# Optimization experiments

Measured on AMD Instinct MI355X. Metric: run time of the kernel, lower is better.

Reference implementation:

```python
import jax, jax.numpy as jnp
import numpy as np

B, N, DIM, HEADS = 4, 1024, 1024, 16
DH = DIM // HEADS
SCALE = 1.0 / np.sqrt(DH)
EPS = 1e-6


def clinear(x, Wr, Wi, br, bi):
    # (a+bi)(Wr+Wi i): real = a Wr^T - b Wi^T, imag = a Wi^T + b Wr^T
    xr, xi = x.real, x.imag
    real = xr @ Wr.T - xi @ Wi.T + br
    imag = xr @ Wi.T + xi @ Wr.T + bi
    return jax.lax.complex(real, imag)


def cln(x, gamma, beta):
    # normalize magnitude over last dim, keep phase
    mag = jnp.abs(x)
    phase = jnp.angle(x)
    mean = jnp.mean(mag, axis=-1, keepdims=True)
    var = jnp.var(mag, axis=-1, keepdims=True)
    nm = (mag - mean) / jnp.sqrt(var + EPS)
    nm = nm * gamma + beta
    return jax.lax.complex(nm * jnp.cos(phase), nm * jnp.sin(phase))


def forward(xr, xi, Wq_r, Wq_i, bq_r, bq_i, Wk_r, Wk_i, bk_r, bk_i,
            Wv_r, Wv_i, bv_r, bv_i, Wo_r, Wo_i, bo_r, bo_i,
            gq, beq, gk, bek, gv, bev):
    x = jax.lax.complex(xr, xi)  # [B,N,D] complex64

    def heads(t):
        return t.reshape(B, N, HEADS, DH).transpose(0, 2, 1, 3)  # [B,H,N,dh]

    Q = heads(cln(clinear(x, Wq_r, Wq_i, bq_r, bq_i), gq, beq))
    K = heads(cln(clinear(x, Wk_r, Wk_i, bk_r, bk_i), gk, bek))
    V = heads(cln(clinear(x, Wv_r, Wv_i, bv_r, bv_i), gv, bev))

    Qf = jnp.fft.fft(Q, axis=2, norm='ortho')
    Kf = jnp.fft.fft(K, axis=2, norm='ortho')
    Vf = jnp.fft.fft(V, axis=2, norm='ortho')

    scores = jnp.einsum('bhnd,bhmd->bhnm', Qf, jnp.conj(Kf)) * SCALE
    attn = jax.nn.softmax(scores.real, axis=-1)  # real-valued softmax
    # attn is real; multiply into complex Vf componentwise
    out_f = jax.lax.complex(jnp.einsum('bhnm,bhmd->bhnd', attn, Vf.real),
                            jnp.einsum('bhnm,bhmd->bhnd', attn, Vf.imag))
    out = jnp.fft.ifft(out_f, axis=2, norm='ortho')
    out = out.transpose(0, 2, 1, 3).reshape(B, N, DIM)
    y = clinear(out, Wo_r, Wo_i, bo_r, bo_i)
    # return real||imag concatenated on last axis (float32 view of complex output)
    return jnp.concatenate([y.real, y.imag], axis=-1)


def setup_inputs() -> dict:
    key = jax.random.key(0)
    ks = jax.random.split(key, 16)
    wscale = np.sqrt(2.0 / (DIM + DIM)).astype(np.float32)
    d = {}
    d['xr'] = jax.random.normal(ks[0], (B, N, DIM), jnp.float32)
    d['xi'] = jax.random.normal(ks[1], (B, N, DIM), jnp.float32)
    i = 2
    for name in ('q', 'k', 'v', 'o'):
        d[f'W{name}_r'] = jax.random.normal(ks[i], (DIM, DIM), jnp.float32) * wscale; i += 1
        d[f'W{name}_i'] = jax.random.normal(ks[i], (DIM, DIM), jnp.float32) * wscale; i += 1
        d[f'b{name}_r'] = jnp.zeros((DIM,), jnp.float32)
        d[f'b{name}_i'] = jnp.zeros((DIM,), jnp.float32)
    for name in ('q', 'k', 'v'):
        d[f'g{name}'] = jnp.ones((DIM,), jnp.float32)
        d[f'be{name}'] = jnp.zeros((DIM,), jnp.float32)
    return d


def reference(xr, xi, Wq_r, Wq_i, bq_r, bq_i, Wk_r, Wk_i, bk_r, bk_i,
              Wv_r, Wv_i, bv_r, bv_i, Wo_r, Wo_i, bo_r, bo_i,
              gq, beq, gk, bek, gv, bev):
    return forward(xr, xi, Wq_r, Wq_i, bq_r, bq_i, Wk_r, Wk_i, bk_r, bk_i,
                   Wv_r, Wv_i, bv_r, bv_i, Wo_r, Wo_i, bo_r, bo_i,
                   gq, beq, gk, bek, gv, bev)
```

## Files before the change

kernel.cpp:

```cpp
#include <hip/hip_runtime.h>
#include <math.h>

#define BB 4
#define NN 1024
#define DIMM 1024
#define HHH 16
#define DHH 64
#define BN 4096
#define EPS_LN 1e-6f

typedef __bf16 bf16_t;
typedef __bf16 bf16x8 __attribute__((ext_vector_type(8)));
typedef float f32x4 __attribute__((ext_vector_type(4)));
typedef float f32x16 __attribute__((ext_vector_type(16)));
#define MFMA16(a, b, c) __builtin_amdgcn_mfma_f32_16x16x32_bf16(a, b, c, 0, 0, 0)
#define MFMA32(a, b, c) __builtin_amdgcn_mfma_f32_32x32x16_bf16(a, b, c, 0, 0, 0)
#define AS1 __attribute__((address_space(1)))
#define AS3 __attribute__((address_space(3)))

__device__ inline unsigned pk2(float a, float b) {
  union { bf16_t h[2]; unsigned u; } c;
  c.h[0] = (bf16_t)a; c.h[1] = (bf16_t)b;
  return c.u;
}
union U16 { uint4 u; bf16x8 v; };

__global__ __launch_bounds__(256) void pack_x(
    const float* __restrict__ xr, const float* __restrict__ xi,
    bf16_t* __restrict__ out)
{
  int t = blockIdx.x * 256 + threadIdx.x;
  size_t e = (size_t)t * 8;
  int row = (int)(e >> 11), col = (int)(e & 2047);
  const float* src = (col < 1024) ? (xr + (size_t)row * 1024 + col)
                                  : (xi + (size_t)row * 1024 + col - 1024);
  float4 a = *(const float4*)src;
  float4 b = *(const float4*)(src + 4);
  bf16x8 o;
  o[0] = (bf16_t)a.x; o[1] = (bf16_t)a.y; o[2] = (bf16_t)a.z; o[3] = (bf16_t)a.w;
  o[4] = (bf16_t)b.x; o[5] = (bf16_t)b.y; o[6] = (bf16_t)b.z; o[7] = (bf16_t)b.w;
  *(bf16x8*)(out + e) = o;
}

__global__ __launch_bounds__(256) void pack_w(
    const float* __restrict__ Wr, const float* __restrict__ Wi,
    const float* __restrict__ br, const float* __restrict__ bi,
    bf16_t* __restrict__ Wcat, float* __restrict__ bcat)
{
  int t = blockIdx.x * 256 + threadIdx.x;
  size_t e = (size_t)t * 8;
  int row = (int)(e >> 11), col = (int)(e & 2047);
  const float* src;
  float sgn = 1.f;
  if (row < 1024) {
    if (col < 1024) src = Wr + (size_t)row * 1024 + col;
    else          { src = Wi + (size_t)row * 1024 + col - 1024; sgn = -1.f; }
  } else {
    int r2 = row - 1024;
    if (col < 1024) src = Wi + (size_t)r2 * 1024 + col;
    else            src = Wr + (size_t)r2 * 1024 + col - 1024;
  }
  float4 a = *(const float4*)src;
  float4 b = *(const float4*)(src + 4);
  bf16x8 o;
  o[0] = (bf16_t)(sgn * a.x); o[1] = (bf16_t)(sgn * a.y);
  o[2] = (bf16_t)(sgn * a.z); o[3] = (bf16_t)(sgn * a.w);
  o[4] = (bf16_t)(sgn * b.x); o[5] = (bf16_t)(sgn * b.y);
  o[6] = (bf16_t)(sgn * b.z); o[7] = (bf16_t)(sgn * b.w);
  *(bf16x8*)(Wcat + e) = o;
  if (e < 2048) {
#pragma unroll
    for (int j = 0; j < 8; ++j) {
      int n = (int)e + j;
      bcat[n] = (n < 1024) ? br[n] : bi[n - 1024];
    }
  }
}

__global__ __launch_bounds__(256) void gemm_bf16(
    const bf16_t* __restrict__ A, const bf16_t* __restrict__ Bt,
    const float* __restrict__ bias,
    float* __restrict__ Cr, float* __restrict__ Ci, int ldc)
{
  __shared__ bf16_t sA[128 * 64];
  __shared__ bf16_t sB[128 * 64];
  const int tid = threadIdx.x;
  const int w = tid >> 6, l = tid & 63;
  const int lo4 = l & 15, hi = l >> 4;
  const int wr = w >> 1, wc = w & 1;
  const int row0 = blockIdx.y * 128, col0 = blockIdx.x * 128;

  const int srow = (l >> 3);
  const int scol = (l & 7) * 8;
  const bf16_t* gA[4];
  const bf16_t* gB[4];
#pragma unroll
  for (int i = 0; i < 4; ++i) {
    int r = (w * 4 + i) * 8 + srow;
    gA[i] = A  + (size_t)(row0 + r) * 2048 + scol;
    gB[i] = Bt + (size_t)(col0 + r) * 2048 + scol;
  }

  f32x4 acc[4][4] = {};
  for (int k0 = 0; k0 < 2048; k0 += 64) {
    __syncthreads();
#pragma unroll
    for (int i = 0; i < 4; ++i) {
      __builtin_amdgcn_global_load_lds((const AS1 void*)(gA[i] + k0),
                                       (AS3 void*)&sA[(w * 4 + i) * 512], 16, 0, 0);
      __builtin_amdgcn_global_load_lds((const AS1 void*)(gB[i] + k0),
                                       (AS3 void*)&sB[(w * 4 + i) * 512], 16, 0, 0);
    }
    __syncthreads();
#pragma unroll
    for (int kk = 0; kk < 2; ++kk) {
      bf16x8 am[4], bn[4];
#pragma unroll
      for (int i = 0; i < 4; ++i)
        am[i] = *(const bf16x8*)&sA[(wr * 64 + i * 16 + lo4) * 64 + kk * 32 + hi * 8];
#pragma unroll
      for (int j = 0; j < 4; ++j)
        bn[j] = *(const bf16x8*)&sB[(wc * 64 + j * 16 + lo4) * 64 + kk * 32 + hi * 8];
#pragma unroll
      for (int i = 0; i < 4; ++i)
#pragma unroll
        for (int j = 0; j < 4; ++j)
          acc[i][j] = MFMA16(am[i], bn[j], acc[i][j]);
    }
  }
  const int colg0 = col0 + wc * 64;
  float* Cp = (colg0 < 1024) ? Cr : Ci;
  const int cb = colg0 & 1023;
#pragma unroll
  for (int i = 0; i < 4; ++i) {
#pragma unroll
    for (int j = 0; j < 4; ++j) {
      float bv = bias[colg0 + j * 16 + lo4];
#pragma unroll
      for (int r = 0; r < 4; ++r) {
        int rowg = row0 + wr * 64 + i * 16 + hi * 4 + r;
        Cp[(size_t)rowg * ldc + cb + j * 16 + lo4] = acc[i][j][r] + bv;
      }
    }
  }
}

__global__ __launch_bounds__(256) void ln_stats(
    const float* __restrict__ re, const float* __restrict__ im,
    float2* __restrict__ st)
{
  __shared__ float red[8];
  const int row = blockIdx.x;
  const int tid = threadIdx.x;
  const float* pr = re + (size_t)row * DIMM;
  const float* pi = im + (size_t)row * DIMM;
  float s = 0.f, s2 = 0.f;
#pragma unroll
  for (int t = 0; t < 4; ++t) {
    int c = tid + t * 256;
    float vr = pr[c], vi = pi[c];
    float mg = sqrtf(vr * vr + vi * vi);
    s += mg; s2 += mg * mg;
  }
#pragma unroll
  for (int o = 32; o; o >>= 1) { s += __shfl_down(s, o); s2 += __shfl_down(s2, o); }
  if ((tid & 63) == 0) { red[tid >> 6] = s; red[4 + (tid >> 6)] = s2; }
  __syncthreads();
  if (tid == 0) {
    float S = red[0] + red[1] + red[2] + red[3];
    float S2 = red[4] + red[5] + red[6] + red[7];
    float mean = S * (1.f / DIMM);
    float var = S2 * (1.f / DIMM) - mean * mean;
    st[row] = make_float2(mean, rsqrtf(var + EPS_LN));
  }
}

#define LIDX(d_, c_) (((d_) << 10) + ((c_) ^ (((c_) >> 5) & 31) ^ (((d_) & 7) << 2)))

__global__ __launch_bounds__(512) void fft_kernel(
    const float* __restrict__ inR, const float* __restrict__ inI,
    bf16_t* __restrict__ outR, bf16_t* __restrict__ outI,
    int in_sb, int in_sh, int in_sn, int in_sd,
    int out_sb, int out_sh, int out_sn,
    float sign, float oscale, int imode, int omode,
    const float2* __restrict__ stats,
    const float* __restrict__ gamma, const float* __restrict__ beta)
{
  __shared__ float lr[8 * 1024], li[8 * 1024];
  __shared__ float2 tw[1024];
  const int tid = threadIdx.x;
  const int dc = blockIdx.x & 7;
  const int bh = blockIdx.x >> 3;
  const int b = bh >> 4, h = bh & 15;
  const float* bR = inR + (size_t)b * in_sb + (size_t)h * in_sh;
  const float* bI = inI + (size_t)b * in_sb + (size_t)h * in_sh;
#pragma unroll
  for (int t = tid; t < 1024; t += 512) {
    float ang = sign * 3.14159265358979323846f * (float)t * (1.f / 512.f);
    float sn, cs;
    __sincosf(ang, &sn, &cs);
    tw[t] = make_float2(cs, sn);
  }
  if (imode == 0) {
    float gg[8], bb[8];
    if (stats) {
#pragma unroll
      for (int ds = 0; ds < 8; ++ds) {
        gg[ds] = gamma[h * DHH + dc * 8 + ds];
        bb[ds] = beta[h * DHH + dc * 8 + ds];
      }
    }
#pragma unroll
    for (int rep = 0; rep < 2; ++rep) {
      int n = tid + rep * 512;
      const float* pR = bR + (size_t)n * in_sn + dc * 8;
      const float* pI = bI + (size_t)n * in_sn + dc * 8;
      union { float4 q[2]; float f[8]; } ur, ui;
      ur.q[0] = *(const float4*)pR;      ur.q[1] = *(const float4*)(pR + 4);
      ui.q[0] = *(const float4*)pI;      ui.q[1] = *(const float4*)(pI + 4);
      if (stats) {
        float2 stv = stats[b * NN + n];
#pragma unroll
        for (int ds = 0; ds < 8; ++ds) {
          float a = ur.f[ds], c2 = ui.f[ds];
          float mag = sqrtf(a * a + c2 * c2);
          float nm = (mag - stv.x) * stv.y * gg[ds] + bb[ds];
          if (mag > 0.f) { float sc = nm / mag; ur.f[ds] = a * sc; ui.f[ds] = c2 * sc; }
          else           { ur.f[ds] = nm; ui.f[ds] = 0.f; }
        }
      }
#pragma unroll
      for (int ds = 0; ds < 8; ++ds) {
        int ax = LIDX(ds, n);
        lr[ax] = ur.f[ds];
        li[ax] = ui.f[ds];
      }
    }
  } else {
    const int ds = tid & 7, nb = tid >> 3;
    const float* pR = bR + (size_t)(dc * 8 + ds) * in_sd + nb * 16;
    const float* pI = bI + (size_t)(dc * 8 + ds) * in_sd + nb * 16;
#pragma unroll
    for (int k = 0; k < 16; k += 4) {
      float4 v = *(const float4*)(pR + k);
      float4 w = *(const float4*)(pI + k);
      int c = nb * 16 + k;
      lr[LIDX(ds, c + 0)] = v.x;  li[LIDX(ds, c + 0)] = w.x;
      lr[LIDX(ds, c + 1)] = v.y;  li[LIDX(ds, c + 1)] = w.y;
      lr[LIDX(ds, c + 2)] = v.z;  li[LIDX(ds, c + 2)] = w.z;
      lr[LIDX(ds, c + 3)] = v.w;  li[LIDX(ds, c + 3)] = w.w;
    }
  }
  __syncthreads();
  const int dsub = tid & 7;
  const int jb = tid >> 3;
  int lq2 = 8;
  for (int st = 0; st < 5; ++st) {
    const int qtr = 1 << lq2;
    const int tmul = 1 << (2 * st);
    for (int jt = 0; jt < 4; ++jt) {
      int j = jb + jt * 64;
      int o = j & (qtr - 1);
      int i0 = ((j >> lq2) << (lq2 + 2)) + o;
      int a0 = LIDX(dsub, i0);
      int a1 = LIDX(dsub, i0 + qtr);
      int a2 = LIDX(dsub, i0 + 2 * qtr);
      int a3 = LIDX(dsub, i0 + 3 * qtr);
      float x0r = lr[a0], x0i = li[a0];
      float x1r = lr[a1], x1i = li[a1];
      float x2r = lr[a2], x2i = li[a2];
      float x3r = lr[a3], x3i = li[a3];
      float ar = x0r + x2r, ai2 = x0i + x2i;
      float br = x0r - x2r, bi  = x0i - x2i;
      float cr = x1r + x3r, ci  = x1i + x3i;
      float dr = x1r - x3r, di  = x1i - x3i;
      float2 t1 = tw[o * tmul];
      float2 t2 = tw[2 * o * tmul];
      float2 t3 = tw[3 * o * tmul];
      lr[a0] = ar + cr;  li[a0] = ai2 + ci;
      float u1r = br - sign * di, u1i = bi + sign * dr;
      lr[a1] = u1r * t1.x - u1i * t1.y;  li[a1] = u1r * t1.y + u1i * t1.x;
      float u2r = ar - cr, u2i = ai2 - ci;
      lr[a2] = u2r * t2.x - u2i * t2.y;  li[a2] = u2r * t2.y + u2i * t2.x;
      float u3r = br + sign * di, u3i = bi - sign * dr;
      lr[a3] = u3r * t3.x - u3i * t3.y;  li[a3] = u3r * t3.y + u3i * t3.x;
    }
    __syncthreads();
    lq2 -= 2;
  }
  bf16_t* oRb = outR + (size_t)b * out_sb + (size_t)h * out_sh;
  bf16_t* oIb = outI + (size_t)b * out_sb + (size_t)h * out_sh;
#pragma unroll
  for (int rep = 0; rep < 2; ++rep) {
    int n = tid + rep * 512;
    int rv2 = __brev((unsigned)n) >> 22;
    int p = ((rv2 & 0x155) << 1) | ((rv2 >> 1) & 0x155);
    float fr[8], fi[8];
#pragma unroll
    for (int ds = 0; ds < 8; ++ds) {
      fr[ds] = lr[LIDX(ds, p)] * oscale;
      fi[ds] = li[LIDX(ds, p)] * oscale;
    }
    if (omode == 1) {
      size_t tb = (size_t)(n >> 5) * 4096;
#pragma unroll
      for (int ds = 0; ds < 8; ++ds) {
        int dch = dc * 8 + ds;
        size_t ga = tb + (size_t)dch * 32 + ((n & 31) ^ (((dch >> 1) & 3) << 3));
        oRb[ga] = (bf16_t)fr[ds];
        oIb[ga] = (bf16_t)fi[ds];
      }
    } else {
      int cb = dc * 8;
      if (omode == 2) cb = (dc ^ (n & 7)) * 8;
      bf16x8 v0, w0;
#pragma unroll
      for (int k = 0; k < 8; ++k) {
        v0[k] = (bf16_t)fr[k];
        w0[k] = (bf16_t)fi[k];
      }
      size_t gb = (size_t)n * out_sn + cb;
      *(bf16x8*)(oRb + gb) = v0;
      *(bf16x8*)(oIb + gb) = w0;
    }
  }
}

__global__ __launch_bounds__(256, 2) void fattn(
    const bf16_t* __restrict__ Qf, const bf16_t* __restrict__ Kfs,
    const bf16_t* __restrict__ Vfs, float* __restrict__ OT)
{
  __shared__ bf16_t K3[3][4096];
  __shared__ bf16_t V3[3][4096];
  const int tid = threadIdx.x;
  const int w = tid >> 6, l = tid & 63;
  const int lq = l & 31;
  const int h = l >> 5;
  const int i = blockIdx.x;
  const int j = i >> 3;
  const int bh = (i & 7) * 8 + (j >> 3);
  const int q0 = (j & 7) * 128 + w * 32;

  bf16x8 bq[8];
  const bf16_t* qp = Qf + ((size_t)bh * NN + q0 + lq) * 128 + h * 8;
#pragma unroll
  for (int kk = 0; kk < 8; ++kk) bq[kk] = *(const bf16x8*)(qp + kk * 16);

  f32x16 o[4] = {};
  float m = -3e38f, ln = 0.f;

  const bf16_t* kg = Kfs + (size_t)bh * 131072 + w * 1024 + l * 8;
  const bf16_t* vg = Vfs + (size_t)bh * 131072 + w * 1024 + l * 8;
  const int kswz = (lq & 7) << 3;
  const int vswz = ((lq >> 1) & 3) << 3;

#pragma unroll
  for (int tt = 0; tt < 2; ++tt) {
    const bf16_t* kt = kg + (size_t)tt * 4096;
    const bf16_t* vt = vg + (size_t)tt * 4096;
#pragma unroll
    for (int ii = 0; ii < 2; ++ii) {
      __builtin_amdgcn_global_load_lds((const AS1 void*)(kt + ii * 512),
                                       (AS3 void*)&K3[tt][w * 1024 + ii * 512], 16, 0, 0);
      __builtin_amdgcn_global_load_lds((const AS1 void*)(vt + ii * 512),
                                       (AS3 void*)&V3[tt][w * 1024 + ii * 512], 16, 0, 0);
    }
  }
  asm volatile("s_waitcnt vmcnt(4)" ::: "memory");
  __builtin_amdgcn_s_barrier();
  __builtin_amdgcn_sched_barrier(0);

  int cur = 0;
  for (int t = 0; t < 32; ++t) {
    if (t < 30) {
      int nb = cur + 2; if (nb >= 3) nb -= 3;
      const bf16_t* kt = kg + (size_t)(t + 2) * 4096;
      const bf16_t* vt = vg + (size_t)(t + 2) * 4096;
#pragma unroll
      for (int ii = 0; ii < 2; ++ii) {
        __builtin_amdgcn_global_load_lds((const AS1 void*)(kt + ii * 512),
                                         (AS3 void*)&K3[nb][w * 1024 + ii * 512], 16, 0, 0);
        __builtin_amdgcn_global_load_lds((const AS1 void*)(vt + ii * 512),
                                         (AS3 void*)&V3[nb][w * 1024 + ii * 512], 16, 0, 0);
      }
    }

    f32x16 s = {};
#pragma unroll
    for (int kk = 0; kk < 8; ++kk) {
      bf16x8 ak = *(const bf16x8*)&K3[cur][lq * 128 + ((kk * 16 + h * 8) ^ kswz)];
      s = MFMA32(ak, bq[kk], s);
    }

    float pmax = s[0];
#pragma unroll
    for (int r = 1; r < 16; ++r) pmax = fmaxf(pmax, s[r]);
    pmax = fmaxf(pmax, __shfl_xor(pmax, 32));
    if (!__all(pmax - m <= 8.f)) {
      float mnew = fmaxf(m, pmax);
      float alpha = __expf(m - mnew);
      m = mnew;
      ln *= alpha;
#pragma unroll
      for (int db = 0; db < 4; ++db)
#pragma unroll
        for (int r = 0; r < 16; ++r) o[db][r] *= alpha;
    }
    float pf[16];
    float rs = 0.f;
#pragma unroll
    for (int r = 0; r < 16; ++r) { pf[r] = __expf(s[r] - m); rs += pf[r]; }
    rs += __shfl_xor(rs, 32);
    ln += rs;

    unsigned pw[8];
#pragma unroll
    for (int ii = 0; ii < 8; ++ii) pw[ii] = pk2(pf[2 * ii], pf[2 * ii + 1]);
    unsigned r0 = (unsigned)__shfl_xor((int)(h ? pw[0] : pw[2]), 32);
    unsigned r1 = (unsigned)__shfl_xor((int)(h ? pw[1] : pw[3]), 32);
    unsigned r2 = (unsigned)__shfl_xor((int)(h ? pw[4] : pw[6]), 32);
    unsigned r3 = (unsigned)__shfl_xor((int)(h ? pw[5] : pw[7]), 32);
    U16 bp0, bp1;
    bp0.u.x = h ? r0 : pw[0];  bp0.u.y = h ? r1 : pw[1];
    bp0.u.z = h ? pw[2] : r0;  bp0.u.w = h ? pw[3] : r1;
    bp1.u.x = h ? r2 : pw[4];  bp1.u.y = h ? r3 : pw[5];
    bp1.u.z = h ? pw[6] : r2;  bp1.u.w = h ? pw[7] : r3;

#pragma unroll
    for (int db = 0; db < 4; ++db) {
      int r = db * 32 + lq;
      bf16x8 av0 = *(const bf16x8*)&V3[cur][r * 32 + ((h * 8) ^ vswz)];
      bf16x8 av1 = *(const bf16x8*)&V3[cur][r * 32 + ((16 + h * 8) ^ vswz)];
      o[db] = MFMA32(av0, bp0.v, o[db]);
      o[db] = MFMA32(av1, bp1.v, o[db]);
    }

    if (t < 31) {
      if (t < 30) asm volatile("s_waitcnt vmcnt(4)" ::: "memory");
      else        asm volatile("s_waitcnt vmcnt(0)" ::: "memory");
      __builtin_amdgcn_s_barrier();
      __builtin_amdgcn_sched_barrier(0);
    }
    cur = (cur == 2) ? 0 : cur + 1;
  }

  float inv = 1.f / ln;
  const size_t otb = (size_t)bh * 128 * NN + q0 + lq;
#pragma unroll
  for (int db = 0; db < 4; ++db)
#pragma unroll
    for (int r = 0; r < 16; ++r) {
      int dl = (r & 3) + 8 * (r >> 2) + 4 * h;
      OT[otb + (size_t)(db * 32 + dl) * NN] = o[db][r] * inv;
    }
}

extern "C" void kernel_launch(void* const* d_in, const int* in_sizes, int n_in,
                              void* d_out, int out_size, void* d_ws, size_t ws_size,
                              hipStream_t stream) {
  const float* xr   = (const float*)d_in[0];
  const float* xi   = (const float*)d_in[1];
  const float* Wqr  = (const float*)d_in[2];
  const float* Wqi  = (const float*)d_in[3];
  const float* bqr  = (const float*)d_in[4];
  const float* bqi  = (const float*)d_in[5];
  const float* Wkr  = (const float*)d_in[6];
  const float* Wki  = (const float*)d_in[7];
  const float* bkr  = (const float*)d_in[8];
  const float* bki  = (const float*)d_in[9];
  const float* Wvr  = (const float*)d_in[10];
  const float* Wvi  = (const float*)d_in[11];
  const float* bvr  = (const float*)d_in[12];
  const float* bvi  = (const float*)d_in[13];
  const float* Wor  = (const float*)d_in[14];
  const float* Woi  = (const float*)d_in[15];
  const float* bor  = (const float*)d_in[16];
  const float* boi  = (const float*)d_in[17];
  const float* gq   = (const float*)d_in[18];
  const float* beq  = (const float*)d_in[19];
  const float* gk   = (const float*)d_in[20];
  const float* bek  = (const float*)d_in[21];
  const float* gv   = (const float*)d_in[22];
  const float* bev  = (const float*)d_in[23];

  char* wp = (char*)d_ws;
  bf16_t* Axaug = (bf16_t*)wp;  wp += (size_t)4096 * 2048 * 2;
  bf16_t* Wcat  = (bf16_t*)wp;  wp += (size_t)2048 * 2048 * 2;
  float*  bcat  = (float*)wp;   wp += (size_t)2048 * 4;
  float2* lnst  = (float2*)wp;  wp += (size_t)4096 * 8;
  float*  Ar    = (float*)wp;   wp += (size_t)4096 * 1024 * 4;
  float*  Ai    = (float*)wp;   wp += (size_t)4096 * 1024 * 4;
  bf16_t* Qf    = (bf16_t*)wp;  wp += (size_t)64 * 1024 * 128 * 2;
  bf16_t* Kf    = (bf16_t*)wp;  wp += (size_t)64 * 1024 * 128 * 2;
  bf16_t* VfT   = (bf16_t*)wp;  wp += (size_t)64 * 1024 * 128 * 2;
  bf16_t* Yaug  = Qf;
  float*  OT    = Ar;

  const dim3 gGemm(16, 32);
  const int gPackX = (4096 * 2048 / 8) / 256;
  const int gPackW = (2048 * 2048 / 8) / 256;
  const int gFft = 64 * 8;
  const int gAtt = 64 * 8;

  pack_x<<<gPackX, 256, 0, stream>>>(xr, xi, Axaug);

  pack_w<<<gPackW, 256, 0, stream>>>(Wqr, Wqi, bqr, bqi, Wcat, bcat);
  gemm_bf16<<<gGemm, 256, 0, stream>>>(Axaug, Wcat, bcat, Ar, Ai, 1024);
  ln_stats<<<BN, 256, 0, stream>>>(Ar, Ai, lnst);
  fft_kernel<<<gFft, 512, 0, stream>>>(Ar, Ai, Qf, Qf + 64,
      NN * DIMM, DHH, DIMM, 1,
      16 * NN * 128, NN * 128, 128,
      -1.0f, 0.03125f * 0.125f, 0, 0, lnst, gq, beq);
  pack_w<<<gPackW, 256, 0, stream>>>(Wkr, Wki, bkr, bki, Wcat, bcat);
  gemm_bf16<<<gGemm, 256, 0, stream>>>(Axaug, Wcat, bcat, Ar, Ai, 1024);
  ln_stats<<<BN, 256, 0, stream>>>(Ar, Ai, lnst);
  fft_kernel<<<gFft, 512, 0, stream>>>(Ar, Ai, Kf, Kf + 64,
      NN * DIMM, DHH, DIMM, 1,
      16 * NN * 128, NN * 128, 128,
      -1.0f, 0.03125f, 0, 2, lnst, gk, bek);
  pack_w<<<gPackW, 256, 0, stream>>>(Wvr, Wvi, bvr, bvi, Wcat, bcat);
  gemm_bf16<<<gGemm, 256, 0, stream>>>(Axaug, Wcat, bcat, Ar, Ai, 1024);
  ln_stats<<<BN, 256, 0, stream>>>(Ar, Ai, lnst);
  fft_kernel<<<gFft, 512, 0, stream>>>(Ar, Ai, VfT, VfT + 2048,
      NN * DIMM, DHH, DIMM, 1,
      16 * 131072, 131072, 0,
      -1.0f, 0.03125f, 0, 1, lnst, gv, bev);
  fattn<<<gAtt, 256, 0, stream>>>(Qf, Kf, VfT, OT);
  fft_kernel<<<gFft, 512, 0, stream>>>(OT, OT + (size_t)64 * NN, Yaug, Yaug + 1024,
      16 * 128 * NN, 128 * NN, 1, NN,
      NN * 2048, 64, 2048,
      +1.0f, 0.03125f, 1, 0, nullptr, nullptr, nullptr);
  float* yout = (float*)d_out;
  pack_w<<<gPackW, 256, 0, stream>>>(Wor, Woi, bor, boi, Wcat, bcat);
  gemm_bf16<<<gGemm, 256, 0, stream>>>(Yaug, Wcat, bcat, yout, yout + 1024, 2048);
}
```

Before: 431.4 us.

## Fuse Q/K/V projections into one GEMM and store intermediates in bf16

Replaces three separate projection GEMMs and three LN-stat passes with a single 6144-wide QKV GEMM and one batched stats kernel. The projection output and the attention output OT are now stored as bf16 instead of fp32, roughly halving intermediate memory traffic for the FFT and stats kernels. This cuts launch count and gives the GEMM a larger grid, which should fill the device better. The cost is extra rounding of pre-layernorm activations and attention outputs to bf16, plus a larger workspace.

```diff
diff --git a/kernel.cpp b/kernel.cpp
--- a/kernel.cpp
+++ b/kernel.cpp
@@ -11,6 +11,7 @@
 
 typedef __bf16 bf16_t;
 typedef __bf16 bf16x8 __attribute__((ext_vector_type(8)));
+typedef __bf16 bf16x4 __attribute__((ext_vector_type(4)));
 typedef float f32x4 __attribute__((ext_vector_type(4)));
 typedef float f32x16 __attribute__((ext_vector_type(16)));
 #define MFMA16(a, b, c) __builtin_amdgcn_mfma_f32_16x16x32_bf16(a, b, c, 0, 0, 0)
@@ -77,6 +78,71 @@
   }
 }
 
+__global__ __launch_bounds__(256) void gemm_qkv(
+    const bf16_t* __restrict__ A, const bf16_t* __restrict__ Bt,
+    const float* __restrict__ bias, bf16_t* __restrict__ C6)
+{
+  __shared__ bf16_t sA[128 * 64];
+  __shared__ bf16_t sB[128 * 64];
+  const int tid = threadIdx.x;
+  const int w = tid >> 6, l = tid & 63;
+  const int lo4 = l & 15, hi = l >> 4;
+  const int wr = w >> 1, wc = w & 1;
+  const int row0 = blockIdx.y * 128, col0 = blockIdx.x * 128;
+
+  const int srow = (l >> 3);
+  const int scol = (l & 7) * 8;
+  const bf16_t* gA[4];
+  const bf16_t* gB[4];
+#pragma unroll
+  for (int i = 0; i < 4; ++i) {
+    int r = (w * 4 + i) * 8 + srow;
+    gA[i] = A  + (size_t)(row0 + r) * 2048 + scol;
+    gB[i] = Bt + (size_t)(col0 + r) * 2048 + scol;
+  }
+
+  f32x4 acc[4][4] = {};
+  for (int k0 = 0; k0 < 2048; k0 += 64) {
+    __syncthreads();
+#pragma unroll
+    for (int i = 0; i < 4; ++i) {
+      __builtin_amdgcn_global_load_lds((const AS1 void*)(gA[i] + k0),
+                                       (AS3 void*)&sA[(w * 4 + i) * 512], 16, 0, 0);
+      __builtin_amdgcn_global_load_lds((const AS1 void*)(gB[i] + k0),
+                                       (AS3 void*)&sB[(w * 4 + i) * 512], 16, 0, 0);
+    }
+    __syncthreads();
+#pragma unroll
+    for (int kk = 0; kk < 2; ++kk) {
+      bf16x8 am[4], bn[4];
+#pragma unroll
+      for (int i = 0; i < 4; ++i)
+        am[i] = *(const bf16x8*)&sA[(wr * 64 + i * 16 + lo4) * 64 + kk * 32 + hi * 8];
+#pragma unroll
+      for (int j = 0; j < 4; ++j)
+        bn[j] = *(const bf16x8*)&sB[(wc * 64 + j * 16 + lo4) * 64 + kk * 32 + hi * 8];
+#pragma unroll
+      for (int i = 0; i < 4; ++i)
+#pragma unroll
+        for (int j = 0; j < 4; ++j)
+          acc[i][j] = MFMA16(am[i], bn[j], acc[i][j]);
+    }
+  }
+  const int colg0 = col0 + wc * 64;
+#pragma unroll
+  for (int i = 0; i < 4; ++i) {
+#pragma unroll
+    for (int j = 0; j < 4; ++j) {
+      float bv = bias[colg0 + j * 16 + lo4];
+#pragma unroll
+      for (int r = 0; r < 4; ++r) {
+        int rowg = row0 + wr * 64 + i * 16 + hi * 4 + r;
+        C6[(size_t)rowg * 6144 + colg0 + j * 16 + lo4] = (bf16_t)(acc[i][j][r] + bv);
+      }
+    }
+  }
+}
+
 __global__ __launch_bounds__(256) void gemm_bf16(
     const bf16_t* __restrict__ A, const bf16_t* __restrict__ Bt,
     const float* __restrict__ bias,
@@ -145,21 +211,22 @@
   }
 }
 
-__global__ __launch_bounds__(256) void ln_stats(
-    const float* __restrict__ re, const float* __restrict__ im,
-    float2* __restrict__ st)
+__global__ __launch_bounds__(256) void ln_stats3(
+    const bf16_t* __restrict__ C6, float2* __restrict__ st)
 {
   __shared__ float red[8];
   const int row = blockIdx.x;
+  const int p = blockIdx.y;
   const int tid = threadIdx.x;
-  const float* pr = re + (size_t)row * DIMM;
-  const float* pi = im + (size_t)row * DIMM;
+  const bf16_t* pr = C6 + (size_t)row * 6144 + p * 2048;
+  const bf16_t* pi = pr + 1024;
+  bf16x4 vr = *(const bf16x4*)(pr + tid * 4);
+  bf16x4 vi = *(const bf16x4*)(pi + tid * 4);
   float s = 0.f, s2 = 0.f;
 #pragma unroll
   for (int t = 0; t < 4; ++t) {
-    int c = tid + t * 256;
-    float vr = pr[c], vi = pi[c];
-    float mg = sqrtf(vr * vr + vi * vi);
+    float a = (float)vr[t], b = (float)vi[t];
+    float mg = sqrtf(a * a + b * b);
     s += mg; s2 += mg * mg;
   }
 #pragma unroll
@@ -171,14 +238,14 @@
     float S2 = red[4] + red[5] + red[6] + red[7];
     float mean = S * (1.f / DIMM);
     float var = S2 * (1.f / DIMM) - mean * mean;
-    st[row] = make_float2(mean, rsqrtf(var + EPS_LN));
+    st[(size_t)p * 4096 + row] = make_float2(mean, rsqrtf(var + EPS_LN));
   }
 }
 
 #define LIDX(d_, c_) (((d_) << 10) + ((c_) ^ (((c_) >> 5) & 31) ^ (((d_) & 7) << 2)))
 
 __global__ __launch_bounds__(512) void fft_kernel(
-    const float* __restrict__ inR, const float* __restrict__ inI,
+    const bf16_t* __restrict__ inR, const bf16_t* __restrict__ inI,
     bf16_t* __restrict__ outR, bf16_t* __restrict__ outI,
     int in_sb, int in_sh, int in_sn, int in_sd,
     int out_sb, int out_sh, int out_sn,
@@ -192,8 +259,8 @@
   const int dc = blockIdx.x & 7;
   const int bh = blockIdx.x >> 3;
   const int b = bh >> 4, h = bh & 15;
-  const float* bR = inR + (size_t)b * in_sb + (size_t)h * in_sh;
-  const float* bI = inI + (size_t)b * in_sb + (size_t)h * in_sh;
+  const bf16_t* bR = inR + (size_t)b * in_sb + (size_t)h * in_sh;
+  const bf16_t* bI = inI + (size_t)b * in_sb + (size_t)h * in_sh;
 #pragma unroll
   for (int t = tid; t < 1024; t += 512) {
     float ang = sign * 3.14159265358979323846f * (float)t * (1.f / 512.f);
@@ -213,42 +280,40 @@
 #pragma unroll
     for (int rep = 0; rep < 2; ++rep) {
       int n = tid + rep * 512;
-      const float* pR = bR + (size_t)n * in_sn + dc * 8;
-      const float* pI = bI + (size_t)n * in_sn + dc * 8;
-      union { float4 q[2]; float f[8]; } ur, ui;
-      ur.q[0] = *(const float4*)pR;      ur.q[1] = *(const float4*)(pR + 4);
-      ui.q[0] = *(const float4*)pI;      ui.q[1] = *(const float4*)(pI + 4);
+      bf16x8 r8 = *(const bf16x8*)(bR + (size_t)n * in_sn + dc * 8);
+      bf16x8 i8 = *(const bf16x8*)(bI + (size_t)n * in_sn + dc * 8);
+      float ur[8], ui[8];
+#pragma unroll
+      for (int ds = 0; ds < 8; ++ds) { ur[ds] = (float)r8[ds]; ui[ds] = (float)i8[ds]; }
       if (stats) {
         float2 stv = stats[b * NN + n];
 #pragma unroll
         for (int ds = 0; ds < 8; ++ds) {
-          float a = ur.f[ds], c2 = ui.f[ds];
+          float a = ur[ds], c2 = ui[ds];
           float mag = sqrtf(a * a + c2 * c2);
           float nm = (mag - stv.x) * stv.y * gg[ds] + bb[ds];
-          if (mag > 0.f) { float sc = nm / mag; ur.f[ds] = a * sc; ui.f[ds] = c2 * sc; }
-          else           { ur.f[ds] = nm; ui.f[ds] = 0.f; }
+          if (mag > 0.f) { float sc = nm / mag; ur[ds] = a * sc; ui[ds] = c2 * sc; }
+          else           { ur[ds] = nm; ui[ds] = 0.f; }
         }
       }
 #pragma unroll
       for (int ds = 0; ds < 8; ++ds) {
         int ax = LIDX(ds, n);
-        lr[ax] = ur.f[ds];
-        li[ax] = ui.f[ds];
+        lr[ax] = ur[ds];
+        li[ax] = ui[ds];
       }
     }
   } else {
     const int ds = tid & 7, nb = tid >> 3;
-    const float* pR = bR + (size_t)(dc * 8 + ds) * in_sd + nb * 16;
-    const float* pI = bI + (size_t)(dc * 8 + ds) * in_sd + nb * 16;
-#pragma unroll
-    for (int k = 0; k < 16; k += 4) {
-      float4 v = *(const float4*)(pR + k);
-      float4 w = *(const float4*)(pI + k);
+    const bf16_t* pR = bR + (size_t)(dc * 8 + ds) * in_sd + nb * 16;
+    const bf16_t* pI = bI + (size_t)(dc * 8 + ds) * in_sd + nb * 16;
+    bf16x8 a0 = *(const bf16x8*)pR, a1 = *(const bf16x8*)(pR + 8);
+    bf16x8 b0 = *(const bf16x8*)pI, b1 = *(const bf16x8*)(pI + 8);
+#pragma unroll
+    for (int k = 0; k < 8; ++k) {
       int c = nb * 16 + k;
-      lr[LIDX(ds, c + 0)] = v.x;  li[LIDX(ds, c + 0)] = w.x;
-      lr[LIDX(ds, c + 1)] = v.y;  li[LIDX(ds, c + 1)] = w.y;
-      lr[LIDX(ds, c + 2)] = v.z;  li[LIDX(ds, c + 2)] = w.z;
-      lr[LIDX(ds, c + 3)] = v.w;  li[LIDX(ds, c + 3)] = w.w;
+      lr[LIDX(ds, c)] = (float)a0[k];       li[LIDX(ds, c)] = (float)b0[k];
+      lr[LIDX(ds, c + 8)] = (float)a1[k];   li[LIDX(ds, c + 8)] = (float)b1[k];
     }
   }
   __syncthreads();
@@ -328,7 +393,7 @@
 
 __global__ __launch_bounds__(256, 2) void fattn(
     const bf16_t* __restrict__ Qf, const bf16_t* __restrict__ Kfs,
-    const bf16_t* __restrict__ Vfs, float* __restrict__ OT)
+    const bf16_t* __restrict__ Vfs, bf16_t* __restrict__ OT)
 {
   __shared__ bf16_t K3[3][4096];
   __shared__ bf16_t V3[3][4096];
@@ -451,7 +516,7 @@
 #pragma unroll
     for (int r = 0; r < 16; ++r) {
       int dl = (r & 3) + 8 * (r >> 2) + 4 * h;
-      OT[otb + (size_t)(db * 32 + dl) * NN] = o[db][r] * inv;
+      OT[otb + (size_t)(db * 32 + dl) * NN] = (bf16_t)(o[db][r] * inv);
     }
 }
 
@@ -485,52 +550,56 @@
 
   char* wp = (char*)d_ws;
   bf16_t* Axaug = (bf16_t*)wp;  wp += (size_t)4096 * 2048 * 2;
-  bf16_t* Wcat  = (bf16_t*)wp;  wp += (size_t)2048 * 2048 * 2;
-  float*  bcat  = (float*)wp;   wp += (size_t)2048 * 4;
-  float2* lnst  = (float2*)wp;  wp += (size_t)4096 * 8;
-  float*  Ar    = (float*)wp;   wp += (size_t)4096 * 1024 * 4;
-  float*  Ai    = (float*)wp;   wp += (size_t)4096 * 1024 * 4;
+  bf16_t* Wcat3 = (bf16_t*)wp;  wp += (size_t)6144 * 2048 * 2;
+  float*  bcat3 = (float*)wp;   wp += (size_t)6144 * 4;
+  float2* lnst3 = (float2*)wp;  wp += (size_t)3 * 4096 * 8;
+  bf16_t* C6    = (bf16_t*)wp;  wp += (size_t)4096 * 6144 * 2;
   bf16_t* Qf    = (bf16_t*)wp;  wp += (size_t)64 * 1024 * 128 * 2;
   bf16_t* Kf    = (bf16_t*)wp;  wp += (size_t)64 * 1024 * 128 * 2;
   bf16_t* VfT   = (bf16_t*)wp;  wp += (size_t)64 * 1024 * 128 * 2;
+  bf16_t* OT    = C6;
   bf16_t* Yaug  = Qf;
-  float*  OT    = Ar;
-
-  const dim3 gGemm(16, 32);
+
+  const dim3 gQKV(48, 32);
+  const dim3 gGemmO(16, 32);
   const int gPackX = (4096 * 2048 / 8) / 256;
   const int gPackW = (2048 * 2048 / 8) / 256;
+  const dim3 gLn(4096, 3);
   const int gFft = 64 * 8;
   const int gAtt = 64 * 8;
 
   pack_x<<<gPackX, 256, 0, stream>>>(xr, xi, Axaug);
-
-  pack_w<<<gPackW, 256, 0, stream>>>(Wqr, Wqi, bqr, bqi, Wcat, bcat);
-  gemm_bf16<<<gGemm, 256, 0, stream>>>(Axaug, Wcat, bcat, Ar, Ai, 1024);
-  ln_stats<<<BN, 256, 0, stream>>>(Ar, Ai, lnst);
-  fft_kernel<<<gFft, 512, 0, stream>>>(Ar, Ai, Qf, Qf + 64,
-      NN * DIMM, DHH, DIMM, 1,
+  pack_w<<<gPackW, 256, 0, stream>>>(Wqr, Wqi, bqr, bqi,
+                                     Wcat3, bcat3);
+  pack_w<<<gPackW, 256, 0, stream>>>(Wkr, Wki, bkr, bki,
+                                     Wcat3 + (size_t)2048 * 2048, bcat3 + 2048);
+  pack_w<<<gPackW, 256, 0, stream>>>(Wvr, Wvi, bvr, bvi,
+                                     Wcat3 + (size_t)4096 * 2048, bcat3 + 4096);
+
+  gemm_qkv<<<gQKV, 256, 0, stream>>>(Axaug, Wcat3, bcat3, C6);
+  ln_stats3<<<gLn, 256, 0, stream>>>(C6, lnst3);
+
+  fft_kernel<<<gFft, 512, 0, stream>>>(C6, C6 + 1024, Qf, Qf + 64,
+      NN * 6144, DHH, 6144, 1,
       16 * NN * 128, NN * 128, 128,
-      -1.0f, 0.03125f * 0.125f, 0, 0, lnst, gq, beq);
-  pack_w<<<gPackW, 256, 0, stream>>>(Wkr, Wki, bkr, bki, Wcat, bcat);
-  gemm_bf16<<<gGemm, 256, 0, stream>>>(Axaug, Wcat, bcat, Ar, Ai, 1024);
-  ln_stats<<<BN, 256, 0, stream>>>(Ar, Ai, lnst);
-  fft_kernel<<<gFft, 512, 0, stream>>>(Ar, Ai, Kf, Kf + 64,
-      NN * DIMM, DHH, DIMM, 1,
+      -1.0f, 0.03125f * 0.125f, 0, 0, lnst3, gq, beq);
+  fft_kernel<<<gFft, 512, 0, stream>>>(C6 + 2048, C6 + 3072, Kf, Kf + 64,
+      NN * 6144, DHH, 6144, 1,
       16 * NN * 128, NN * 128, 128,
-      -1.0f, 0.03125f, 0, 2, lnst, gk, bek);
-  pack_w<<<gPackW, 256, 0, stream>>>(Wvr, Wvi, bvr, bvi, Wcat, bcat);
-  gemm_bf16<<<gGemm, 256, 0, stream>>>(Axaug, Wcat, bcat, Ar, Ai, 1024);
-  ln_stats<<<BN, 256, 0, stream>>>(Ar, Ai, lnst);
-  fft_kernel<<<gFft, 512, 0, stream>>>(Ar, Ai, VfT, VfT + 2048,
-      NN * DIMM, DHH, DIMM, 1,
+      -1.0f, 0.03125f, 0, 2, lnst3 + 4096, gk, bek);
+  fft_kernel<<<gFft, 512, 0, stream>>>(C6 + 4096, C6 + 5120, VfT, VfT + 2048,
+      NN * 6144, DHH, 6144, 1,
       16 * 131072, 131072, 0,
-      -1.0f, 0.03125f, 0, 1, lnst, gv, bev);
+      -1.0f, 0.03125f, 0, 1, lnst3 + 8192, gv, bev);
+
   fattn<<<gAtt, 256, 0, stream>>>(Qf, Kf, VfT, OT);
+
   fft_kernel<<<gFft, 512, 0, stream>>>(OT, OT + (size_t)64 * NN, Yaug, Yaug + 1024,
       16 * 128 * NN, 128 * NN, 1, NN,
       NN * 2048, 64, 2048,
       +1.0f, 0.03125f, 1, 0, nullptr, nullptr, nullptr);
+
   float* yout = (float*)d_out;
-  pack_w<<<gPackW, 256, 0, stream>>>(Wor, Woi, bor, boi, Wcat, bcat);
-  gemm_bf16<<<gGemm, 256, 0, stream>>>(Yaug, Wcat, bcat, yout, yout + 1024, 2048);
-}
+  pack_w<<<gPackW, 256, 0, stream>>>(Wor, Woi, bor, boi, Wcat3, bcat3);
+  gemm_bf16<<<gGemmO, 256, 0, stream>>>(Yaug, Wcat3, bcat3, yout, yout + 1024, 2048);
+}
```

New measurement: 410.1 us. 1.05x faster.
